# Kernel tuning notes

Hardware: AMD Instinct MI355X
Metric: run time of the kernel (lower is better)

Reference implementation:

```python
import jax, jax.numpy as jnp
import numpy as np

EPS = 1e-8

def _l2norm(x):
    return x / (jnp.linalg.norm(x, axis=-1, keepdims=True) + EPS)

def setup_inputs() -> dict:
    key = jax.random.key(0)
    k1, k2, k3, k4, k5, k6 = jax.random.split(key, 6)
    NQ, NB, NF = 16384, 128, 64
    HD = 2 * NF
    Q = jax.random.normal(k1, (NQ, HD), dtype=jnp.float32)
    reference_angles = jax.random.uniform(k2, (NF,), dtype=jnp.float32) * 2.0 * np.pi
    probes = jax.random.normal(k3, (NB, HD), dtype=jnp.float32)
    # params: perturb around the torch inits (log(e-1), zeros, zeros) for a non-degenerate test
    init_val = float(np.log(np.e - 1.0))
    q_weights_raw = init_val + 0.1 * jax.random.normal(k4, (NB, NF), dtype=jnp.float32)
    q_magnitude_weights = 0.1 * jax.random.normal(k5, (NB, NF), dtype=jnp.float32)
    q_bias = 0.1 * jax.random.normal(k6, (NB,), dtype=jnp.float32)
    return {"Q": Q, "reference_angles": reference_angles, "probes": probes,
            "q_weights_raw": q_weights_raw, "q_magnitude_weights": q_magnitude_weights,
            "q_bias": q_bias}

def reference(Q, reference_angles, probes, q_weights_raw, q_magnitude_weights, q_bias):
    NF = reference_angles.shape[0]
    # --- shared probe layer: L2 normalize then RoPE-rotate (front/back real/imag layout)
    pn = _l2norm(probes)                      # (B, 2F)
    pr, pi = pn[:, :NF], pn[:, NF:]
    c, s = jnp.cos(reference_angles), jnp.sin(reference_angles)
    P_real = pr * c - pi * s                  # (B, F)
    P_imag = pr * s + pi * c
    # --- distance-based scorer
    Qn = _l2norm(Q)                           # (Nq, 2F)
    Q_real, Q_imag = Qn[:, :NF], Qn[:, NF:]
    err_r = P_real[None, :, :] - Q_real[:, None, :]   # (Nq, B, F)
    err_i = P_imag[None, :, :] - Q_imag[:, None, :]
    distance = jnp.sqrt(err_r ** 2 + err_i ** 2 + EPS)
    eff_w = -jax.nn.softplus(q_weights_raw)           # (B, F), negative weights
    distance_term = jnp.einsum('qbf,bf->qb', distance, eff_w)
    Q_mag = jnp.sqrt(Q_real ** 2 + Q_imag ** 2 + EPS)  # (Nq, F)
    magnitude_term = Q_mag @ q_magnitude_weights.T     # (Nq, B)
    return distance_term + magnitude_term + q_bias
```

## Files before the change

### kernel.cpp

```cpp
#include <hip/hip_runtime.h>

#define NQ 16384
#define NB 128
#define NF 64
#define HD 128
#define EPSF 1e-8f
#define BTILE 8

__device__ __forceinline__ float wave_allreduce_sum(float v) {
    #pragma unroll
    for (int m = 1; m < 64; m <<= 1) v += __shfl_xor(v, m, 64);
    return v;
}

__global__ __launch_bounds__(64) void build_table_kernel(
    const float* __restrict__ probes,
    const float* __restrict__ angles,
    const float* __restrict__ qw,
    const float* __restrict__ mw,
    float4* __restrict__ tableD,
    float* __restrict__ tableM) {
    const int b = blockIdx.x;
    const int lane = threadIdx.x;
    float p0 = probes[b * HD + lane];
    float p1 = probes[b * HD + 64 + lane];
    float ss = wave_allreduce_sum(p0 * p0 + p1 * p1);
    float inv = 1.0f / (sqrtf(ss) + EPSF);
    float pr = p0 * inv, pi = p1 * inv;
    float ang = angles[lane];
    float c = cosf(ang), s = sinf(ang);
    float Pr = pr * c - pi * s;
    float Pi = pr * s + pi * c;
    float x = qw[b * NF + lane];
    float sp = (x > 0.0f) ? (x + log1pf(expf(-x))) : log1pf(expf(x));
    tableD[lane * NB + b] = make_float4(-2.0f * Pr, -2.0f * Pi,
                                        Pr * Pr + Pi * Pi + EPSF, -sp);
    tableM[lane * NB + b] = mw[b * NF + lane];
}

__global__ __launch_bounds__(256) void build_qvals_kernel(
    const float* __restrict__ Q,
    float4* __restrict__ qvals) {
    const int q = blockIdx.x * 4 + (threadIdx.x >> 6);
    const int lane = threadIdx.x & 63;
    float a = Q[q * HD + lane];
    float c2 = Q[q * HD + 64 + lane];
    float ss = wave_allreduce_sum(a * a + c2 * c2);
    float inv = 1.0f / (sqrtf(ss) + EPSF);
    float Qr = a * inv, Qi = c2 * inv;
    float B = Qr * Qr + Qi * Qi;
    float Qm = sqrtf(B + EPSF);
    qvals[(size_t)q * NF + lane] = make_float4(Qr, Qi, B, Qm);
}

__global__ __launch_bounds__(256, 4) void main_kernel(
    const float4* __restrict__ tableD,
    const float* __restrict__ tableM,
    const float4* __restrict__ qvals,
    const float* __restrict__ bias,
    float* __restrict__ out) {
    __shared__ __align__(16) float4 ldsD[NF * BTILE];
    __shared__ __align__(16) float  ldsM[NF * BTILE];
    const int bt   = blockIdx.x & 15;
    const int qblk = blockIdx.x >> 4;
    const int wave = threadIdx.x >> 6;
    const int lane = threadIdx.x & 63;
    const int q = qblk * 256 + wave * 64 + lane;

    #pragma unroll
    for (int i = 0; i < 2; ++i) {
        int idx = threadIdx.x + i * 256;
        int f = idx >> 3, bb = idx & 7;
        ldsD[idx] = tableD[f * NB + bt * BTILE + bb];
        ldsM[idx] = tableM[f * NB + bt * BTILE + bb];
    }
    __syncthreads();

    float acc[BTILE];
    #pragma unroll
    for (int i = 0; i < BTILE; ++i) acc[i] = 0.0f;

    const float4* qp = qvals + (size_t)q * NF;

    #pragma unroll 8
    for (int f = 0; f < NF; ++f) {
        float4 qv = qp[f];
        float4 tma = *(const float4*)&ldsM[f * 8];
        float4 tmb = *(const float4*)&ldsM[f * 8 + 4];
        const float* tm = &tma.x;
        #pragma unroll
        for (int bb = 0; bb < BTILE; ++bb) {
            float4 td = ldsD[f * 8 + bb];
            float t = td.z + qv.z;
            t = fmaf(td.y, qv.y, t);
            t = fmaf(td.x, qv.x, t);
            t = fmaxf(t, 0.0f);
            float d = __builtin_amdgcn_sqrtf(t);
            float w = (bb < 4) ? (&tma.x)[bb] : (&tmb.x)[bb - 4];
            acc[bb] = fmaf(td.w, d, acc[bb]);
            acc[bb] = fmaf(w, qv.w, acc[bb]);
        }
    }

    #pragma unroll
    for (int bb = 0; bb < BTILE; ++bb) acc[bb] += bias[bt * BTILE + bb];
    float* op = out + (size_t)q * NB + bt * BTILE;
    *(float4*)op       = make_float4(acc[0], acc[1], acc[2], acc[3]);
    *(float4*)(op + 4) = make_float4(acc[4], acc[5], acc[6], acc[7]);
}

extern "C" void kernel_launch(void* const* d_in, const int* in_sizes, int n_in,
                              void* d_out, int out_size, void* d_ws, size_t ws_size,
                              hipStream_t stream) {
    const float* Q      = (const float*)d_in[0];
    const float* angles = (const float*)d_in[1];
    const float* probes = (const float*)d_in[2];
    const float* qw     = (const float*)d_in[3];
    const float* mw     = (const float*)d_in[4];
    const float* bias   = (const float*)d_in[5];
    float* out = (float*)d_out;

    char* ws = (char*)d_ws;
    float4* tableD = (float4*)ws;
    float*  tableM = (float*)(ws + NF * NB * sizeof(float4));
    float4* qvals  = (float4*)(ws + NF * NB * sizeof(float4)
                                  + NF * NB * sizeof(float));

    build_table_kernel<<<NB, 64, 0, stream>>>(probes, angles, qw, mw, tableD, tableM);
    build_qvals_kernel<<<NQ / 4, 256, 0, stream>>>(Q, qvals);
    main_kernel<<<(NQ / 256) * (NB / BTILE), 256, 0, stream>>>(tableD, tableM, qvals, bias, out);
}
```

Measured before the change: 113.4 us.

## Merge prep kernels and read tile-contiguous table directly without LDS staging

Measured after the change: 110.1 us. 3.0% less time.

```diff
diff --git a/kernel.cpp b/kernel.cpp
--- a/kernel.cpp
+++ b/kernel.cpp
@@ -6,99 +6,89 @@
 #define HD 128
 #define EPSF 1e-8f
 #define BTILE 8
+#define NBT (NB / BTILE)
 
-__device__ __forceinline__ float wave_allreduce_sum(float v) {
-    #pragma unroll
-    for (int m = 1; m < 64; m <<= 1) v += __shfl_xor(v, m, 64);
-    return v;
-}
+struct FRow {
+    float4 d[BTILE];
+    float  m[BTILE];
+};
 
-__global__ __launch_bounds__(64) void build_table_kernel(
+__global__ __launch_bounds__(256) void prep_kernel(
+    const float* __restrict__ Q,
     const float* __restrict__ probes,
     const float* __restrict__ angles,
     const float* __restrict__ qw,
     const float* __restrict__ mw,
-    float4* __restrict__ tableD,
-    float* __restrict__ tableM) {
-    const int b = blockIdx.x;
-    const int lane = threadIdx.x;
-    float p0 = probes[b * HD + lane];
-    float p1 = probes[b * HD + 64 + lane];
-    float ss = wave_allreduce_sum(p0 * p0 + p1 * p1);
-    float inv = 1.0f / (sqrtf(ss) + EPSF);
-    float pr = p0 * inv, pi = p1 * inv;
-    float ang = angles[lane];
-    float c = cosf(ang), s = sinf(ang);
-    float Pr = pr * c - pi * s;
-    float Pi = pr * s + pi * c;
-    float x = qw[b * NF + lane];
-    float sp = (x > 0.0f) ? (x + log1pf(expf(-x))) : log1pf(expf(x));
-    tableD[lane * NB + b] = make_float4(-2.0f * Pr, -2.0f * Pi,
-                                        Pr * Pr + Pi * Pi + EPSF, -sp);
-    tableM[lane * NB + b] = mw[b * NF + lane];
-}
-
-__global__ __launch_bounds__(256) void build_qvals_kernel(
-    const float* __restrict__ Q,
-    float4* __restrict__ qvals) {
-    const int q = blockIdx.x * 4 + (threadIdx.x >> 6);
-    const int lane = threadIdx.x & 63;
-    float a = Q[q * HD + lane];
-    float c2 = Q[q * HD + 64 + lane];
-    float ss = wave_allreduce_sum(a * a + c2 * c2);
-    float inv = 1.0f / (sqrtf(ss) + EPSF);
-    float Qr = a * inv, Qi = c2 * inv;
-    float B = Qr * Qr + Qi * Qi;
-    float Qm = sqrtf(B + EPSF);
-    qvals[(size_t)q * NF + lane] = make_float4(Qr, Qi, B, Qm);
+    float4* __restrict__ qvals,
+    FRow* __restrict__ tab) {
+    if (blockIdx.x < 2048) {
+        const int q  = blockIdx.x * 8 + (threadIdx.x >> 5);
+        const int sl = threadIdx.x & 31;
+        const float2* Q2 = (const float2*)Q;
+        float2 a = Q2[q * 64 + sl];
+        float2 c = Q2[q * 64 + 32 + sl];
+        float ss = a.x * a.x + a.y * a.y + c.x * c.x + c.y * c.y;
+        #pragma unroll
+        for (int m = 1; m < 32; m <<= 1) ss += __shfl_xor(ss, m);
+        float inv = 1.0f / (sqrtf(ss) + EPSF);
+        float Qr0 = a.x * inv, Qr1 = a.y * inv;
+        float Qi0 = c.x * inv, Qi1 = c.y * inv;
+        float B0 = Qr0 * Qr0 + Qi0 * Qi0;
+        float B1 = Qr1 * Qr1 + Qi1 * Qi1;
+        qvals[(size_t)q * NF + 2 * sl]     = make_float4(Qr0, Qi0, B0, sqrtf(B0 + EPSF));
+        qvals[(size_t)q * NF + 2 * sl + 1] = make_float4(Qr1, Qi1, B1, sqrtf(B1 + EPSF));
+    } else {
+        const int b    = (blockIdx.x - 2048) * 4 + (threadIdx.x >> 6);
+        const int lane = threadIdx.x & 63;
+        float p0 = probes[b * HD + lane];
+        float p1 = probes[b * HD + 64 + lane];
+        float ss = p0 * p0 + p1 * p1;
+        #pragma unroll
+        for (int m = 1; m < 64; m <<= 1) ss += __shfl_xor(ss, m);
+        float inv = 1.0f / (sqrtf(ss) + EPSF);
+        float pr = p0 * inv, pi = p1 * inv;
+        float ang = angles[lane];
+        float cc = cosf(ang), sn = sinf(ang);
+        float Pr = pr * cc - pi * sn;
+        float Pi = pr * sn + pi * cc;
+        float x = qw[b * NF + lane];
+        float sp = (x > 0.0f) ? (x + log1pf(expf(-x))) : log1pf(expf(x));
+        FRow* r = &tab[(b >> 3) * NF + lane];
+        r->d[b & 7] = make_float4(-2.0f * Pr, -2.0f * Pi, Pr * Pr + Pi * Pi + EPSF, -sp);
+        r->m[b & 7] = mw[b * NF + lane];
+    }
 }
 
 __global__ __launch_bounds__(256, 4) void main_kernel(
-    const float4* __restrict__ tableD,
-    const float* __restrict__ tableM,
+    const FRow* __restrict__ tab,
     const float4* __restrict__ qvals,
     const float* __restrict__ bias,
     float* __restrict__ out) {
-    __shared__ __align__(16) float4 ldsD[NF * BTILE];
-    __shared__ __align__(16) float  ldsM[NF * BTILE];
-    const int bt   = blockIdx.x & 15;
-    const int qblk = blockIdx.x >> 4;
-    const int wave = threadIdx.x >> 6;
-    const int lane = threadIdx.x & 63;
-    const int q = qblk * 256 + wave * 64 + lane;
+    const int bt   = blockIdx.x & (NBT - 1);
+    const int qblk = blockIdx.x / NBT;
+    const int q = qblk * 256 + (threadIdx.x >> 6) * 64 + (threadIdx.x & 63);
 
-    #pragma unroll
-    for (int i = 0; i < 2; ++i) {
-        int idx = threadIdx.x + i * 256;
-        int f = idx >> 3, bb = idx & 7;
-        ldsD[idx] = tableD[f * NB + bt * BTILE + bb];
-        ldsM[idx] = tableM[f * NB + bt * BTILE + bb];
-    }
-    __syncthreads();
+    const FRow* __restrict__ tr = tab + bt * NF;
+    const float4* __restrict__ qp = qvals + (size_t)q * NF;
 
     float acc[BTILE];
     #pragma unroll
     for (int i = 0; i < BTILE; ++i) acc[i] = 0.0f;
 
-    const float4* qp = qvals + (size_t)q * NF;
-
-    #pragma unroll 8
+    #pragma unroll 4
     for (int f = 0; f < NF; ++f) {
         float4 qv = qp[f];
-        float4 tma = *(const float4*)&ldsM[f * 8];
-        float4 tmb = *(const float4*)&ldsM[f * 8 + 4];
-        const float* tm = &tma.x;
         #pragma unroll
         for (int bb = 0; bb < BTILE; ++bb) {
-            float4 td = ldsD[f * 8 + bb];
+            float4 td = tr[f].d[bb];
+            float tm  = tr[f].m[bb];
             float t = td.z + qv.z;
             t = fmaf(td.y, qv.y, t);
             t = fmaf(td.x, qv.x, t);
             t = fmaxf(t, 0.0f);
             float d = __builtin_amdgcn_sqrtf(t);
-            float w = (bb < 4) ? (&tma.x)[bb] : (&tmb.x)[bb - 4];
             acc[bb] = fmaf(td.w, d, acc[bb]);
-            acc[bb] = fmaf(w, qv.w, acc[bb]);
+            acc[bb] = fmaf(tm, qv.w, acc[bb]);
         }
     }
 
@@ -121,12 +111,9 @@
     float* out = (float*)d_out;
 
     char* ws = (char*)d_ws;
-    float4* tableD = (float4*)ws;
-    float*  tableM = (float*)(ws + NF * NB * sizeof(float4));
-    float4* qvals  = (float4*)(ws + NF * NB * sizeof(float4)
-                                  + NF * NB * sizeof(float));
+    FRow*   tab   = (FRow*)ws;
+    float4* qvals = (float4*)(ws + NBT * NF * sizeof(FRow));
 
-    build_table_kernel<<<NB, 64, 0, stream>>>(probes, angles, qw, mw, tableD, tableM);
-    build_qvals_kernel<<<NQ / 4, 256, 0, stream>>>(Q, qvals);
-    main_kernel<<<(NQ / 256) * (NB / BTILE), 256, 0, stream>>>(tableD, tableM, qvals, bias, out);
+    prep_kernel<<<2048 + NB / 4, 256, 0, stream>>>(Q, probes, angles, qw, mw, qvals, tab);
+    main_kernel<<<(NQ / 256) * NBT, 256, 0, stream>>>(tab, qvals, bias, out);
 }
```
